# Kernel tuning notes

Hardware: AMD Instinct MI355X
Metric: run time of the kernel (lower is better)

The kernel has to match this reference:

```python
import jax, jax.numpy as jnp
import numpy as np
from jax import lax

VOCAB, NUM_CLASSES = 21128, 53
EMB, FILT, K = 128, 128, 3
B, L = 512, 512


def setup_inputs() -> dict:
    key = jax.random.key(0)
    ks = jax.random.split(key, 8)
    char_ids = jax.random.randint(ks[0], (B, L), 0, VOCAB, dtype=jnp.int64 if jax.config.jax_enable_x64 else jnp.int32)
    pos_e1 = jax.random.randint(ks[1], (B,), 0, L - 1, dtype=jnp.int32)
    pos_e2 = jax.random.randint(ks[2], (B,), 0, L - 1, dtype=jnp.int32)
    emb_table = jax.random.normal(ks[3], (VOCAB, EMB), dtype=jnp.float32) * 0.02
    emb_table = emb_table.at[0].set(0.0)  # padding_idx=0
    conv_w = jax.random.normal(ks[4], (FILT, EMB, K), dtype=jnp.float32) * (1.0 / np.sqrt(EMB * K))
    conv_b = jax.random.normal(ks[5], (FILT,), dtype=jnp.float32) * 0.01
    fc_w = jax.random.normal(ks[6], (NUM_CLASSES, FILT * 3), dtype=jnp.float32) * (1.0 / np.sqrt(FILT * 3))
    fc_b = jax.random.normal(ks[7], (NUM_CLASSES,), dtype=jnp.float32) * 0.01
    return {"char_ids": char_ids, "pos_e1": pos_e1, "pos_e2": pos_e2,
            "emb_table": emb_table, "conv_w": conv_w, "conv_b": conv_b,
            "fc_w": fc_w, "fc_b": fc_b}


def reference(char_ids, pos_e1, pos_e2, emb_table, conv_w, conv_b, fc_w, fc_b):
    b, seq = char_ids.shape
    x = emb_table[char_ids]                      # (b, L, E)
    x = jnp.transpose(x, (0, 2, 1))              # (b, E, L)
    conv_out = lax.conv_general_dilated(
        x, conv_w, window_strides=(1,), padding=[(K // 2, K // 2)],
        dimension_numbers=("NCH", "OIH", "NCH"))
    conv_out = jax.nn.relu(conv_out + conv_b[None, :, None])  # (b, F, L)

    # sort + clip entity boundaries, replicate e1==e2 -> e2=e1+1 adjustment
    e1 = jnp.clip(jnp.minimum(pos_e1, pos_e2), 0, seq)
    e2 = jnp.clip(jnp.maximum(pos_e1, pos_e2), 0, seq)
    e2 = jnp.where(e1 == e2, jnp.minimum(e1 + 1, seq), e2)

    idx = jnp.arange(seq)[None, :]               # (1, L)
    m1 = idx < jnp.maximum(e1, 1)[:, None]       # [:e1] or [:1] if e1==0
    m2 = (idx >= e1[:, None]) & (idx < e2[:, None])
    m3 = idx >= jnp.minimum(e2, seq - 1)[:, None]  # [e2:] or last col if e2==L

    neg = jnp.float32(-jnp.inf)
    def seg_max(mask):
        return jnp.max(jnp.where(mask[:, None, :], conv_out, neg), axis=-1)  # (b, F)

    pooled = jnp.concatenate([seg_max(m1), seg_max(m2), seg_max(m3)], axis=-1)  # (b, 3F)
    return pooled @ fc_w.T + fc_b
```

## Files before the change

kernel.cpp:

```cpp
#include <hip/hip_runtime.h>
#include <stdint.h>

#define VOCAB 21128
#define NUMC  53
#define EMB   128
#define SEQ   512
#define BATCH 512

typedef __bf16 bf16x8 __attribute__((ext_vector_type(8)));
typedef float f32x4 __attribute__((ext_vector_type(4)));
typedef __attribute__((address_space(3))) void lds_void;
typedef const __attribute__((address_space(1))) void glob_void;

__device__ __forceinline__ unsigned int f2bf1(float f) {
    union { float f; unsigned int u; } v; v.f = f;
    return (v.u + 0x7FFFu + ((v.u >> 16) & 1u)) >> 16;
}
__device__ __forceinline__ unsigned int pack2(float a, float b) {
    return f2bf1(a) | (f2bf1(b) << 16);
}

__global__ void prep_kernel(const float* __restrict__ emb, const float* __restrict__ cw,
                            unsigned short* __restrict__ Tb, unsigned short* __restrict__ Wp) {
    int idx = blockIdx.x * blockDim.x + threadIdx.x;
    const int n8 = VOCAB * EMB / 8;
    if (idx < n8) {
        const float4* src = (const float4*)emb + (size_t)idx * 2;
        float4 a = src[0], b = src[1];
        uint4 o;
        o.x = pack2(a.x, a.y);
        o.y = pack2(a.z, a.w);
        o.z = pack2(b.x, b.y);
        o.w = pack2(b.z, b.w);
        *(uint4*)(Tb + (size_t)idx * 8) = o;
    }
    if (idx < 12 * 8 * 64 * 8) {
        int j = idx & 7, l = (idx >> 3) & 63, g = (idx >> 9) & 7, s = idx >> 12;
        int kk = s * 32 + (l >> 4) * 8 + j;
        int f = g * 16 + (l & 15);
        int tap = kk >> 7, e = kk & 127;
        Wp[idx] = (unsigned short)f2bf1(cw[(f * EMB + e) * 3 + tap]);
    }
}

__launch_bounds__(256, 4)
__global__ void pcnn_tile(const int* __restrict__ cid, const int* __restrict__ p1,
                          const int* __restrict__ p2,
                          const unsigned short* __restrict__ Tb,
                          const unsigned short* __restrict__ Wp,
                          float* __restrict__ Pd) {
    __shared__ __align__(16) unsigned short xs[130 * 128];

    const int bx   = blockIdx.x;
    const int b    = bx >> 2;
    const int tq   = bx & 3;
    const int tid  = threadIdx.x;
    const int lane = tid & 63;
    const int w    = tid >> 6;
    const int wm   = w & 1;
    const int wn2  = w >> 1;
    const int quad = lane >> 4;
    const int lc   = lane & 15;

    const int* crow = cid + (size_t)b * SEQ;
    const char* TbB = (const char*)Tb;
    char* xsB = (char*)xs;

#pragma unroll
    for (int i = 0; i < 9; ++i) {
        int task = tid + 256 * i;
        if (task < 2080) {
            int r = task >> 4, c = task & 15;
            int p = tq * 128 + r - 1;
            unsigned int id = (p >= 0 && p < SEQ) ? (unsigned int)crow[p] : 0u;
            int cs = c ^ (r & 15);
            __builtin_amdgcn_global_load_lds(
                (glob_void*)(TbB + (size_t)id * 256u + cs * 16),
                (lds_void*)(xsB + task * 16), 16, 0, 0);
        }
    }

    int e1 = min(p1[b], p2[b]);
    int e2 = max(p1[b], p2[b]);
    if (e1 == e2) e2 = min(e1 + 1, SEQ);
    const int e1m = max(e1, 1);

    __syncthreads();

    f32x4 acc[4][4];
#pragma unroll
    for (int mt = 0; mt < 4; ++mt)
#pragma unroll
        for (int nt = 0; nt < 4; ++nt)
            acc[mt][nt] = (f32x4){0.f, 0.f, 0.f, 0.f};

#pragma unroll
    for (int s = 0; s < 12; ++s) {
        const int tap = s >> 2;
        const int q   = (s & 3) * 4 + quad;
        const int cs  = q ^ ((lc + tap) & 15);
        bf16x8 bfr[4];
#pragma unroll
        for (int nt = 0; nt < 4; ++nt)
            bfr[nt] = *(const bf16x8*)(Wp + (size_t)((s * 8 + wn2 * 4 + nt) * 64 + lane) * 8);
#pragma unroll
        for (int mt = 0; mt < 4; ++mt) {
            int r = wm * 64 + mt * 16 + lc + tap;
            bf16x8 a = *(const bf16x8*)(xs + r * 128 + cs * 8);
#pragma unroll
            for (int nt = 0; nt < 4; ++nt)
                acc[mt][nt] = __builtin_amdgcn_mfma_f32_16x16x32_bf16(a, bfr[nt], acc[mt][nt], 0, 0, 0);
        }
    }

    float smax[3][4];
#pragma unroll
    for (int s3 = 0; s3 < 3; ++s3)
#pragma unroll
        for (int nt = 0; nt < 4; ++nt) smax[s3][nt] = -1e30f;

#pragma unroll
    for (int mt = 0; mt < 4; ++mt)
#pragma unroll
        for (int reg = 0; reg < 4; ++reg) {
            int p = tq * 128 + wm * 64 + mt * 16 + quad * 4 + reg;
            float a0 = (p < e1m) ? 0.f : -2e30f;
            float a1 = (p >= e1 && p < e2) ? 0.f : -2e30f;
            float a2 = (p >= e2) ? 0.f : -2e30f;
#pragma unroll
            for (int nt = 0; nt < 4; ++nt) {
                float v = acc[mt][nt][reg];
                smax[0][nt] = fmaxf(smax[0][nt], v + a0);
                smax[1][nt] = fmaxf(smax[1][nt], v + a1);
                smax[2][nt] = fmaxf(smax[2][nt], v + a2);
            }
        }

#pragma unroll
    for (int s3 = 0; s3 < 3; ++s3)
#pragma unroll
        for (int nt = 0; nt < 4; ++nt) {
            float v = smax[s3][nt];
            v = fmaxf(v, __shfl_xor(v, 16));
            v = fmaxf(v, __shfl_xor(v, 32));
            smax[s3][nt] = v;
        }
    if (lane < 16) {
        float* pd = Pd + (((size_t)b * 4 + tq) * 2 + wm) * 384;
#pragma unroll
        for (int s3 = 0; s3 < 3; ++s3)
#pragma unroll
            for (int nt = 0; nt < 4; ++nt)
                pd[s3 * 128 + wn2 * 64 + nt * 16 + lc] = smax[s3][nt];
    }
}

__launch_bounds__(256)
__global__ void pcnn_combine(const float* __restrict__ Pd, const float* __restrict__ cb,
                             const float* __restrict__ fcw, const float* __restrict__ fcb,
                             float* __restrict__ out) {
    __shared__ float pooled[384];
    __shared__ float fcred[NUMC][4];
    const int b = blockIdx.x;
    const int tid = threadIdx.x;

    for (int j = tid; j < 384; j += 256) {
        const float* pp = Pd + (size_t)b * 8 * 384 + j;
        float m0 = fmaxf(pp[0 * 384], pp[1 * 384]);
        float m1 = fmaxf(pp[2 * 384], pp[3 * 384]);
        float m2 = fmaxf(pp[4 * 384], pp[5 * 384]);
        float m3 = fmaxf(pp[6 * 384], pp[7 * 384]);
        float m = fmaxf(fmaxf(m0, m1), fmaxf(m2, m3));
        pooled[j] = fmaxf(m + cb[j & 127], 0.f);
    }
    __syncthreads();

    if (tid < 212) {
        int c = tid >> 2, q = tid & 3;
        const float* wrow = fcw + (size_t)c * 384 + q * 96;
        const float* pp   = pooled + q * 96;
        float sum = 0.f;
#pragma unroll 8
        for (int i = 0; i < 96; ++i) sum += wrow[i] * pp[i];
        fcred[c][q] = sum;
    }
    __syncthreads();
    if (tid < NUMC)
        out[(size_t)b * NUMC + tid] =
            fcred[tid][0] + fcred[tid][1] + fcred[tid][2] + fcred[tid][3] + fcb[tid];
}

extern "C" void kernel_launch(void* const* d_in, const int* in_sizes, int n_in,
                              void* d_out, int out_size, void* d_ws, size_t ws_size,
                              hipStream_t stream) {
    const int*   cid = (const int*)d_in[0];
    const int*   p1  = (const int*)d_in[1];
    const int*   p2  = (const int*)d_in[2];
    const float* emb = (const float*)d_in[3];
    const float* cw  = (const float*)d_in[4];
    const float* cb  = (const float*)d_in[5];
    const float* fcw = (const float*)d_in[6];
    const float* fcb = (const float*)d_in[7];
    float* out = (float*)d_out;

    unsigned short* Tb = (unsigned short*)d_ws;
    unsigned short* Wp = (unsigned short*)((char*)d_ws + (size_t)VOCAB * EMB * 2);
    float*          Pd = (float*)((char*)d_ws + (size_t)VOCAB * EMB * 2 + 98304);

    const int n8 = VOCAB * EMB / 8;
    const int prep_threads = 256;
    const int prep_blocks  = (n8 + prep_threads - 1) / prep_threads;
    prep_kernel<<<prep_blocks, prep_threads, 0, stream>>>(emb, cw, Tb, Wp);
    pcnn_tile<<<BATCH * 4, 256, 0, stream>>>(cid, p1, p2, Tb, Wp, Pd);
    pcnn_combine<<<BATCH, 256, 0, stream>>>(Pd, cb, fcw, fcb, out);
}
```

Before: 115.6 us.

## Fuse tile and combine kernels into per-batch block with double-buffered staging

```diff
diff --git a/kernel.cpp b/kernel.cpp
--- a/kernel.cpp
+++ b/kernel.cpp
@@ -43,17 +43,21 @@
     }
 }
 
-__launch_bounds__(256, 4)
-__global__ void pcnn_tile(const int* __restrict__ cid, const int* __restrict__ p1,
-                          const int* __restrict__ p2,
-                          const unsigned short* __restrict__ Tb,
-                          const unsigned short* __restrict__ Wp,
-                          float* __restrict__ Pd) {
-    __shared__ __align__(16) unsigned short xs[130 * 128];
-
-    const int bx   = blockIdx.x;
-    const int b    = bx >> 2;
-    const int tq   = bx & 3;
+__launch_bounds__(256, 2)
+__global__ void pcnn_fused(const int* __restrict__ cid, const int* __restrict__ p1,
+                           const int* __restrict__ p2,
+                           const unsigned short* __restrict__ Tb,
+                           const unsigned short* __restrict__ Wp,
+                           const float* __restrict__ cb,
+                           const float* __restrict__ fcw,
+                           const float* __restrict__ fcb,
+                           float* __restrict__ out) {
+    __shared__ __align__(16) unsigned short xs[2][130 * 128];
+    __shared__ float pstage[2][3][128];
+    __shared__ float pooled[384];
+    __shared__ float fcred[NUMC][4];
+
+    const int b    = blockIdx.x;
     const int tid  = threadIdx.x;
     const int lane = tid & 63;
     const int w    = tid >> 6;
@@ -66,75 +70,89 @@
     const char* TbB = (const char*)Tb;
     char* xsB = (char*)xs;
 
-#pragma unroll
-    for (int i = 0; i < 9; ++i) {
-        int task = tid + 256 * i;
-        if (task < 2080) {
-            int r = task >> 4, c = task & 15;
-            int p = tq * 128 + r - 1;
-            unsigned int id = (p >= 0 && p < SEQ) ? (unsigned int)crow[p] : 0u;
-            int cs = c ^ (r & 15);
-            __builtin_amdgcn_global_load_lds(
-                (glob_void*)(TbB + (size_t)id * 256u + cs * 16),
-                (lds_void*)(xsB + task * 16), 16, 0, 0);
+    auto STAGE = [&](int buf, int tq) {
+#pragma unroll
+        for (int i = 0; i < 9; ++i) {
+            int task = tid + 256 * i;
+            if (task < 2080) {
+                int r = task >> 4, c = task & 15;
+                int p = tq * 128 + r - 1;
+                unsigned int id = (p >= 0 && p < SEQ) ? (unsigned int)crow[p] : 0u;
+                int cs = c ^ (r & 15);
+                __builtin_amdgcn_global_load_lds(
+                    (glob_void*)(TbB + (size_t)id * 256u + cs * 16),
+                    (lds_void*)(xsB + buf * (130 * 128 * 2) + task * 16), 16, 0, 0);
+            }
         }
-    }
+    };
+
+    STAGE(0, 0);
 
     int e1 = min(p1[b], p2[b]);
     int e2 = max(p1[b], p2[b]);
     if (e1 == e2) e2 = min(e1 + 1, SEQ);
     const int e1m = max(e1, 1);
 
-    __syncthreads();
-
-    f32x4 acc[4][4];
-#pragma unroll
-    for (int mt = 0; mt < 4; ++mt)
-#pragma unroll
-        for (int nt = 0; nt < 4; ++nt)
-            acc[mt][nt] = (f32x4){0.f, 0.f, 0.f, 0.f};
-
-#pragma unroll
-    for (int s = 0; s < 12; ++s) {
-        const int tap = s >> 2;
-        const int q   = (s & 3) * 4 + quad;
-        const int cs  = q ^ ((lc + tap) & 15);
-        bf16x8 bfr[4];
-#pragma unroll
-        for (int nt = 0; nt < 4; ++nt)
-            bfr[nt] = *(const bf16x8*)(Wp + (size_t)((s * 8 + wn2 * 4 + nt) * 64 + lane) * 8);
-#pragma unroll
-        for (int mt = 0; mt < 4; ++mt) {
-            int r = wm * 64 + mt * 16 + lc + tap;
-            bf16x8 a = *(const bf16x8*)(xs + r * 128 + cs * 8);
+    float smax[3][4];
+#pragma unroll
+    for (int s3 = 0; s3 < 3; ++s3)
+#pragma unroll
+        for (int nt = 0; nt < 4; ++nt) smax[s3][nt] = -1e30f;
+
+    int cur = 0;
+    __syncthreads();
+
+    for (int tq = 0; tq < 4; ++tq) {
+        if (tq < 3) STAGE(cur ^ 1, tq + 1);
+
+        const unsigned short* xsc = xs[0] + cur * (130 * 128);
+
+        f32x4 acc[4][4];
+#pragma unroll
+        for (int mt = 0; mt < 4; ++mt)
 #pragma unroll
             for (int nt = 0; nt < 4; ++nt)
-                acc[mt][nt] = __builtin_amdgcn_mfma_f32_16x16x32_bf16(a, bfr[nt], acc[mt][nt], 0, 0, 0);
-        }
-    }
-
-    float smax[3][4];
-#pragma unroll
-    for (int s3 = 0; s3 < 3; ++s3)
-#pragma unroll
-        for (int nt = 0; nt < 4; ++nt) smax[s3][nt] = -1e30f;
-
-#pragma unroll
-    for (int mt = 0; mt < 4; ++mt)
-#pragma unroll
-        for (int reg = 0; reg < 4; ++reg) {
-            int p = tq * 128 + wm * 64 + mt * 16 + quad * 4 + reg;
-            float a0 = (p < e1m) ? 0.f : -2e30f;
-            float a1 = (p >= e1 && p < e2) ? 0.f : -2e30f;
-            float a2 = (p >= e2) ? 0.f : -2e30f;
-#pragma unroll
-            for (int nt = 0; nt < 4; ++nt) {
-                float v = acc[mt][nt][reg];
-                smax[0][nt] = fmaxf(smax[0][nt], v + a0);
-                smax[1][nt] = fmaxf(smax[1][nt], v + a1);
-                smax[2][nt] = fmaxf(smax[2][nt], v + a2);
+                acc[mt][nt] = (f32x4){0.f, 0.f, 0.f, 0.f};
+
+#pragma unroll
+        for (int s = 0; s < 12; ++s) {
+            const int tap = s >> 2;
+            const int q   = (s & 3) * 4 + quad;
+            const int cs  = q ^ ((lc + tap) & 15);
+            bf16x8 bfr[4];
+#pragma unroll
+            for (int nt = 0; nt < 4; ++nt)
+                bfr[nt] = *(const bf16x8*)(Wp + (size_t)((s * 8 + wn2 * 4 + nt) * 64 + lane) * 8);
+#pragma unroll
+            for (int mt = 0; mt < 4; ++mt) {
+                int r = wm * 64 + mt * 16 + lc + tap;
+                bf16x8 a = *(const bf16x8*)(xsc + r * 128 + cs * 8);
+#pragma unroll
+                for (int nt = 0; nt < 4; ++nt)
+                    acc[mt][nt] = __builtin_amdgcn_mfma_f32_16x16x32_bf16(a, bfr[nt], acc[mt][nt], 0, 0, 0);
             }
         }
+
+#pragma unroll
+        for (int mt = 0; mt < 4; ++mt)
+#pragma unroll
+            for (int reg = 0; reg < 4; ++reg) {
+                int p = tq * 128 + wm * 64 + mt * 16 + quad * 4 + reg;
+                float a0 = (p < e1m) ? 0.f : -2e30f;
+                float a1 = (p >= e1 && p < e2) ? 0.f : -2e30f;
+                float a2 = (p >= e2) ? 0.f : -2e30f;
+#pragma unroll
+                for (int nt = 0; nt < 4; ++nt) {
+                    float v = acc[mt][nt][reg];
+                    smax[0][nt] = fmaxf(smax[0][nt], v + a0);
+                    smax[1][nt] = fmaxf(smax[1][nt], v + a1);
+                    smax[2][nt] = fmaxf(smax[2][nt], v + a2);
+                }
+            }
+
+        __syncthreads();
+        cur ^= 1;
+    }
 
 #pragma unroll
     for (int s3 = 0; s3 < 3; ++s3)
@@ -146,32 +164,18 @@
             smax[s3][nt] = v;
         }
     if (lane < 16) {
-        float* pd = Pd + (((size_t)b * 4 + tq) * 2 + wm) * 384;
 #pragma unroll
         for (int s3 = 0; s3 < 3; ++s3)
 #pragma unroll
             for (int nt = 0; nt < 4; ++nt)
-                pd[s3 * 128 + wn2 * 64 + nt * 16 + lc] = smax[s3][nt];
-    }
-}
-
-__launch_bounds__(256)
-__global__ void pcnn_combine(const float* __restrict__ Pd, const float* __restrict__ cb,
-                             const float* __restrict__ fcw, const float* __restrict__ fcb,
-                             float* __restrict__ out) {
-    __shared__ float pooled[384];
-    __shared__ float fcred[NUMC][4];
-    const int b = blockIdx.x;
-    const int tid = threadIdx.x;
+                pstage[wm][s3][wn2 * 64 + nt * 16 + lc] = smax[s3][nt];
+    }
+    __syncthreads();
 
     for (int j = tid; j < 384; j += 256) {
-        const float* pp = Pd + (size_t)b * 8 * 384 + j;
-        float m0 = fmaxf(pp[0 * 384], pp[1 * 384]);
-        float m1 = fmaxf(pp[2 * 384], pp[3 * 384]);
-        float m2 = fmaxf(pp[4 * 384], pp[5 * 384]);
-        float m3 = fmaxf(pp[6 * 384], pp[7 * 384]);
-        float m = fmaxf(fmaxf(m0, m1), fmaxf(m2, m3));
-        pooled[j] = fmaxf(m + cb[j & 127], 0.f);
+        int s3 = j >> 7, f = j & 127;
+        float m = fmaxf(pstage[0][s3][f], pstage[1][s3][f]);
+        pooled[j] = fmaxf(m + cb[f], 0.f);
     }
     __syncthreads();
 
@@ -205,12 +209,10 @@
 
     unsigned short* Tb = (unsigned short*)d_ws;
     unsigned short* Wp = (unsigned short*)((char*)d_ws + (size_t)VOCAB * EMB * 2);
-    float*          Pd = (float*)((char*)d_ws + (size_t)VOCAB * EMB * 2 + 98304);
 
     const int n8 = VOCAB * EMB / 8;
     const int prep_threads = 256;
     const int prep_blocks  = (n8 + prep_threads - 1) / prep_threads;
     prep_kernel<<<prep_blocks, prep_threads, 0, stream>>>(emb, cw, Tb, Wp);
-    pcnn_tile<<<BATCH * 4, 256, 0, stream>>>(cid, p1, p2, Tb, Wp, Pd);
-    pcnn_combine<<<BATCH, 256, 0, stream>>>(Pd, cb, fcw, fcb, out);
-}
+    pcnn_fused<<<BATCH, 256, 0, stream>>>(cid, p1, p2, Tb, Wp, cb, fcw, fcb, out);
+}
```

New measurement: 181.7 us. 57.2% more time.
